# Kernel tuning notes

Measured on AMD Instinct MI355X. Metric: run time of the kernel, lower is better.

Reference implementation:

```python
import jax, jax.numpy as jnp
import numpy as np

B, C, COUT, L, K = 16, 64, 64, 16384, 3
STRIDE, PAD, DIL, G, DG = 1, 1, 1, 1, 1
LOUT = (L + 2 * PAD - DIL * (K - 1) - 1) // STRIDE + 1


def _conv1d(x, w, b, pad, groups):
    # x: [B, Cin, L], w: [Cout, Cin/groups, k] (torch Conv1d layout)
    y = jax.lax.conv_general_dilated(
        x, w, window_strides=(1,), padding=[(pad, pad)],
        dimension_numbers=('NCH', 'OIH', 'NCH'), feature_group_count=groups)
    return y + b[None, :, None]


def setup_inputs() -> dict:
    key = jax.random.key(0)
    k = jax.random.split(key, 11)
    s = jnp.float32(0.02)  # module init: normal(0, 0.02)
    return {
        'x': jax.random.normal(k[0], (B, C, L), jnp.float32),
        'w_off_dw': jax.random.normal(k[1], (C, 1, 7), jnp.float32) * s,
        'b_off_dw': jax.random.normal(k[2], (C,), jnp.float32) * s,
        'w_off_pw': jax.random.normal(k[3], (G * DG * K, C, 1), jnp.float32) * s,
        'b_off_pw': jax.random.normal(k[4], (G * DG * K,), jnp.float32) * s,
        'w_msk_dw': jax.random.normal(k[5], (C, 1, 7), jnp.float32) * s,
        'b_msk_dw': jax.random.normal(k[6], (C,), jnp.float32) * s,
        'w_msk_pw': jax.random.normal(k[7], (G * DG * K, C, 1), jnp.float32) * s,
        'b_msk_pw': jax.random.normal(k[8], (G * DG * K,), jnp.float32) * s,
        'weight': jax.random.normal(k[9], (COUT, C // G, K), jnp.float32) * s,
        'bias': jax.random.normal(k[10], (COUT,), jnp.float32) * s,
    }


def _deform_conv1d(x, w_off_dw, b_off_dw, w_off_pw, b_off_pw,
                   w_msk_dw, b_msk_dw, w_msk_pw, b_msk_pw, weight, bias):
    # offset / modulation-mask branches: depthwise k=7 conv -> 1x1 conv
    offset = _conv1d(_conv1d(x, w_off_dw, b_off_dw, 3, C), w_off_pw, b_off_pw, 0, 1)  # [B, G*DG*K, Lout]
    mask = jax.nn.sigmoid(_conv1d(_conv1d(x, w_msk_dw, b_msk_dw, 3, C), w_msk_pw, b_msk_pw, 0, 1))

    cpd = C // (G * DG)  # channels per deformable group
    off = jnp.repeat(offset.reshape(B, G * DG, K, LOUT), cpd, axis=1)  # [B, C, K, Lout]
    msk = jnp.repeat(mask.reshape(B, G * DG, K, LOUT), cpd, axis=1)

    base = jnp.arange(LOUT, dtype=x.dtype) * STRIDE - PAD  # [Lout]
    kpos = jnp.arange(K, dtype=x.dtype) * DIL              # [K]
    p = base[None, :] + kpos[:, None]                       # [K, Lout]
    p = p[None, None] + off                                 # fractional sample positions [B, C, K, Lout]

    i0 = jnp.floor(p)
    frac = p - i0
    i0i = i0.astype(jnp.int32)
    i1i = i0i + 1

    xb = jnp.broadcast_to(x[:, :, None, :], (B, C, K, L))
    x0 = jnp.take_along_axis(xb, jnp.clip(i0i, 0, L - 1), axis=-1)
    x1 = jnp.take_along_axis(xb, jnp.clip(i1i, 0, L - 1), axis=-1)
    v0 = ((i0i >= 0) & (i0i < L)).astype(x.dtype)  # zero padding outside
    v1 = ((i1i >= 0) & (i1i < L)).astype(x.dtype)

    # linear interpolation + mask modulation
    val = ((1.0 - frac) * x0 * v0 + frac * x1 * v1) * msk  # [B, C, K, Lout]

    # grouped contraction over (in-channels-per-group, kernel taps)
    out = jnp.einsum('bgikl,goik->bgol',
                     val.reshape(B, G, C // G, K, LOUT),
                     weight.reshape(G, COUT // G, C // G, K))
    return out.reshape(B, COUT, LOUT) + bias[None, :, None]


def reference(x, w_off_dw, b_off_dw, w_off_pw, b_off_pw,
              w_msk_dw, b_msk_dw, w_msk_pw, b_msk_pw, weight, bias):
    return _deform_conv1d(x, w_off_dw, b_off_dw, w_off_pw, b_off_pw,
                          w_msk_dw, b_msk_dw, w_msk_pw, b_msk_pw, weight, bias)
```

## Files before the change

kernel.cpp:

```cpp
#include <hip/hip_runtime.h>
#include <cstdint>

#define LX 16384
#define NB 16
#define LT 64
#define HALO 8
#define XI (LT + 2*HALO)
#define XPD 36
#define HPD 36

typedef __attribute__((ext_vector_type(2))) _Float16 h2;
typedef __attribute__((ext_vector_type(8))) _Float16 h8;
typedef __attribute__((ext_vector_type(4))) unsigned u4;
typedef __attribute__((ext_vector_type(4))) float f4;

static __device__ __forceinline__ h2 u2h(unsigned u) {
    union { unsigned u; h2 h; } v; v.u = u; return v.h;
}
static __device__ __forceinline__ unsigned h2u(h2 h) {
    union { h2 h; unsigned u; } v; v.h = h; return v.u;
}
static __device__ __forceinline__ unsigned pkrtz(float a, float b) {
    auto r = __builtin_amdgcn_cvt_pkrtz(a, b);
    union { decltype(r) h; unsigned u; } v; v.h = r;
    return v.u;
}

__global__ void prep_kernel(const float* __restrict__ weight,
                            const float* __restrict__ b_off_pw, const float* __restrict__ w_off_pw,
                            const float* __restrict__ b_off_dw,
                            const float* __restrict__ b_msk_pw, const float* __restrict__ w_msk_pw,
                            const float* __restrict__ b_msk_dw,
                            const float* __restrict__ w_off_dw, const float* __restrict__ w_msk_dw,
                            short* __restrict__ A, float* __restrict__ beff,
                            unsigned* __restrict__ dwt2, unsigned* __restrict__ pwt2) {
    int bid = blockIdx.x;
    int t = threadIdx.x;
    if (bid < 48) {
        int idx = bid * 256 + t;
        int k = idx >> 12;
        int o = (idx >> 6) & 63, c = idx & 63;
        union { _Float16 h; short s; } v;
        v.h = (_Float16)weight[o * 192 + c * 3 + k];
        A[idx] = v.s;
    } else {
        for (int idx = t; idx < 448; idx += 256) {
            int br = idx / 224, r2 = idx - br * 224;
            int j = r2 >> 5, cp = r2 & 31;
            const float* src = br ? w_msk_dw : w_off_dw;
            h2 h; h[0] = (_Float16)src[(2 * cp) * 7 + j]; h[1] = (_Float16)src[(2 * cp + 1) * 7 + j];
            dwt2[idx] = h2u(h);
        }
        if (t < 192) {
            int br = t / 96, r2 = t - br * 96;
            int m = r2 >> 5, cp = r2 & 31;
            const float* src = br ? w_msk_pw : w_off_pw;
            h2 h; h[0] = (_Float16)src[m * 64 + 2 * cp]; h[1] = (_Float16)src[m * 64 + 2 * cp + 1];
            pwt2[t] = h2u(h);
        }
        if (t < 6) {
            int br = t / 3, m = t % 3;
            const float* pw = br ? w_msk_pw : w_off_pw;
            const float* bd = br ? b_msk_dw : b_off_dw;
            const float* bp = br ? b_msk_pw : b_off_pw;
            float s = bp[m];
            for (int c = 0; c < 64; ++c) s += pw[m * 64 + c] * bd[c];
            beff[t] = s;
        }
    }
}

__launch_bounds__(256, 3)
__global__ void deform_main(const float* __restrict__ x,
                            const float* __restrict__ bias,
                            const short* __restrict__ A,
                            const float* __restrict__ beff,
                            const unsigned* __restrict__ dwt2_g,
                            const unsigned* __restrict__ pwt2_g,
                            float* __restrict__ out) {
    __shared__ __align__(16) unsigned xdw[XI * XPD];
    __shared__ __align__(16) unsigned Hdw[3 * XI * HPD];
    __shared__ __align__(16) unsigned dwt2[448];
    __shared__ __align__(16) unsigned pwt2[192];
    __shared__ unsigned kl_wp[3][64];
    __shared__ int      kl_li[3][64];
    __shared__ float bias_l[64];
    __shared__ float beff_l[8];

    const int t = threadIdx.x;
    const int l0 = blockIdx.x * LT;
    const int b = blockIdx.y;

    const float* xb = x + (size_t)b * (64 * LX);
    #pragma unroll
    for (int s = 0; s < 3; ++s) {
        int p = t + 256 * s;
        if (p < 640) {
            int cp = p & 31, up = p >> 5;
            int g4 = l0 - HALO + up * 4;
            f4 v0 = {0.f, 0.f, 0.f, 0.f}, v1 = {0.f, 0.f, 0.f, 0.f};
            if ((unsigned)g4 < (unsigned)LX) {
                v0 = *(const f4*)(xb + (size_t)(2 * cp) * LX + g4);
                v1 = *(const f4*)(xb + (size_t)(2 * cp + 1) * LX + g4);
            }
            #pragma unroll
            for (int d = 0; d < 4; ++d) {
                int i = up * 4 + d;
                int pc = ((cp >> 3) + i) & 3;
                xdw[i * XPD + pc * 8 + (cp & 7)] = pkrtz(v0[d], v1[d]);
            }
        }
    }
    for (int idx = t; idx < 448; idx += 256) dwt2[idx] = dwt2_g[idx];
    if (t < 192) pwt2[t] = pwt2_g[t];
    if (t < 64) bias_l[t] = bias[t];
    if (t < 6)  beff_l[t] = beff[t];

    const int lane = t & 63;
    const int wv = t >> 6;
    const int r = lane & 15, q = lane >> 4;
    const int m0 = wv * 16;
    h8 afr[6];
    {
        const h8* Ap = (const h8*)A;
        #pragma unroll
        for (int k = 0; k < 3; ++k)
            #pragma unroll
            for (int ks = 0; ks < 2; ++ks)
                afr[k * 2 + ks] = Ap[(k * 64 + m0 + r) * 8 + ks * 4 + q];
    }
    __syncthreads();

    {
        const int l = t >> 2, cc = t & 3;
        h2 so2[8], sm2[8];
        #pragma unroll
        for (int m = 0; m < 8; ++m) { so2[m] = (h2)(_Float16)0; sm2[m] = (h2)(_Float16)0; }
        #pragma unroll
        for (int j = 0; j < 7; ++j) {
            int i = l + 5 + j;
            const unsigned* xr = &xdw[i * XPD + (((cc + i) & 3) << 3)];
            u4 xa = *(const u4*)xr;
            u4 xb2 = *(const u4*)(xr + 4);
            const unsigned* wo = &dwt2[j * 32 + cc * 8];
            const unsigned* wm = &dwt2[224 + j * 32 + cc * 8];
            u4 woa = *(const u4*)wo, wob = *(const u4*)(wo + 4);
            u4 wma = *(const u4*)wm, wmb = *(const u4*)(wm + 4);
            #pragma unroll
            for (int m = 0; m < 4; ++m) {
                so2[m]     += u2h(xa[m])  * u2h(woa[m]);
                so2[m + 4] += u2h(xb2[m]) * u2h(wob[m]);
                sm2[m]     += u2h(xa[m])  * u2h(wma[m]);
                sm2[m + 4] += u2h(xb2[m]) * u2h(wmb[m]);
            }
        }
        float po[3] = {0.f, 0.f, 0.f}, pm[3] = {0.f, 0.f, 0.f};
        #pragma unroll
        for (int m3 = 0; m3 < 3; ++m3) {
            const unsigned* p0 = &pwt2[m3 * 32 + cc * 8];
            const unsigned* p1 = &pwt2[96 + m3 * 32 + cc * 8];
            u4 a0 = *(const u4*)p0, a1 = *(const u4*)(p0 + 4);
            u4 b0 = *(const u4*)p1, b1 = *(const u4*)(p1 + 4);
            #pragma unroll
            for (int m = 0; m < 4; ++m) {
                po[m3] = __builtin_amdgcn_fdot2(so2[m],     u2h(a0[m]), po[m3], false);
                po[m3] = __builtin_amdgcn_fdot2(so2[m + 4], u2h(a1[m]), po[m3], false);
                pm[m3] = __builtin_amdgcn_fdot2(sm2[m],     u2h(b0[m]), pm[m3], false);
                pm[m3] = __builtin_amdgcn_fdot2(sm2[m + 4], u2h(b1[m]), pm[m3], false);
            }
        }
        #pragma unroll
        for (int d = 1; d <= 2; d <<= 1) {
            #pragma unroll
            for (int m3 = 0; m3 < 3; ++m3) {
                po[m3] += __shfl_xor(po[m3], d);
                pm[m3] += __shfl_xor(pm[m3], d);
            }
        }
        if (cc < 3) {
            int k = cc;
            float off = (k == 0 ? po[0] : k == 1 ? po[1] : po[2]) + beff_l[k];
            float z   = (k == 0 ? pm[0] : k == 1 ? pm[1] : pm[2]) + beff_l[3 + k];
            float msk = 1.0f / (1.0f + __expf(-z));
            float p = (float)(l0 + l - 1 + k) + off;
            float fl = floorf(p);
            int i0 = (int)fl, i1 = i0 + 1;
            float fr = p - fl;
            int li0 = i0 - l0 + HALO, li1 = li0 + 1;
            float w0 = (((unsigned)i0 < (unsigned)LX) && ((unsigned)li0 < (unsigned)XI)) ? (1.0f - fr) * msk : 0.0f;
            float w1 = (((unsigned)i1 < (unsigned)LX) && ((unsigned)li1 < (unsigned)XI)) ? fr * msk : 0.0f;
            li0 = min(max(li0, 0), XI - 2);
            kl_wp[k][l] = pkrtz(w0, w1);
            kl_li[k][l] = li0;
        }
    }

    {
        h8 bfr[10];
        #pragma unroll
        for (int n = 0; n < 5; ++n)
            #pragma unroll
            for (int ks = 0; ks < 2; ++ks) {
                int i = n * 16 + r;
                int pc = ((2 * ks + (q >> 1)) + i) & 3;
                bfr[n * 2 + ks] = *(const h8*)&xdw[i * XPD + pc * 8 + (q & 1) * 4];
            }
        #pragma unroll
        for (int k = 0; k < 3; ++k) {
            #pragma unroll
            for (int n = 0; n < 5; ++n) {
                f4 acc = {0.f, 0.f, 0.f, 0.f};
                acc = __builtin_amdgcn_mfma_f32_16x16x32_f16(afr[k * 2 + 0], bfr[n * 2 + 0], acc, 0, 0, 0);
                acc = __builtin_amdgcn_mfma_f32_16x16x32_f16(afr[k * 2 + 1], bfr[n * 2 + 1], acc, 0, 0, 0);
                int i = n * 16 + r;
                int pc = (wv + i) & 3;
                unsigned* dst = &Hdw[(k * XI + i) * HPD + pc * 8 + 2 * q];
                dst[0] = pkrtz(acc[0], acc[1]);
                dst[1] = pkrtz(acc[2], acc[3]);
            }
        }
    }
    __syncthreads();

    {
        const int l = t & 63, og = t >> 6;
        float acc[16];
        #pragma unroll
        for (int oi = 0; oi < 16; ++oi) acc[oi] = bias_l[og * 16 + oi];
        #pragma unroll
        for (int k = 0; k < 3; ++k) {
            h2 wph = u2h(kl_wp[k][l]);
            int li0 = kl_li[k][l];
            int b0 = (k * XI + li0) * HPD + (((og + li0) & 3) << 3);
            int b1 = (k * XI + li0 + 1) * HPD + (((og + li0 + 1) & 3) << 3);
            u4 r0a = *(const u4*)&Hdw[b0], r0b = *(const u4*)&Hdw[b0 + 4];
            u4 r1a = *(const u4*)&Hdw[b1], r1b = *(const u4*)&Hdw[b1 + 4];
            #pragma unroll
            for (int m = 0; m < 4; ++m) {
                unsigned dA0 = __builtin_amdgcn_perm(r1a[m], r0a[m], 0x05040100u);
                unsigned dA1 = __builtin_amdgcn_perm(r1a[m], r0a[m], 0x07060302u);
                acc[2 * m]     = __builtin_amdgcn_fdot2(u2h(dA0), wph, acc[2 * m], false);
                acc[2 * m + 1] = __builtin_amdgcn_fdot2(u2h(dA1), wph, acc[2 * m + 1], false);
                unsigned dB0 = __builtin_amdgcn_perm(r1b[m], r0b[m], 0x05040100u);
                unsigned dB1 = __builtin_amdgcn_perm(r1b[m], r0b[m], 0x07060302u);
                acc[8 + 2 * m]     = __builtin_amdgcn_fdot2(u2h(dB0), wph, acc[8 + 2 * m], false);
                acc[8 + 2 * m + 1] = __builtin_amdgcn_fdot2(u2h(dB1), wph, acc[8 + 2 * m + 1], false);
            }
        }
        float* ob = out + ((size_t)b * 64 + og * 16) * LX + l0 + l;
        #pragma unroll
        for (int oi = 0; oi < 16; ++oi) ob[(size_t)oi * LX] = acc[oi];
    }
}

extern "C" void kernel_launch(void* const* d_in, const int* in_sizes, int n_in,
                              void* d_out, int out_size, void* d_ws, size_t ws_size,
                              hipStream_t stream) {
    const float* x        = (const float*)d_in[0];
    const float* w_off_dw = (const float*)d_in[1];
    const float* b_off_dw = (const float*)d_in[2];
    const float* w_off_pw = (const float*)d_in[3];
    const float* b_off_pw = (const float*)d_in[4];
    const float* w_msk_dw = (const float*)d_in[5];
    const float* b_msk_dw = (const float*)d_in[6];
    const float* w_msk_pw = (const float*)d_in[7];
    const float* b_msk_pw = (const float*)d_in[8];
    const float* weight   = (const float*)d_in[9];
    const float* bias     = (const float*)d_in[10];
    float* out = (float*)d_out;

    short*    A    = (short*)d_ws;
    float*    beff = (float*)((char*)d_ws + 24576);
    unsigned* dwt2 = (unsigned*)((char*)d_ws + 24608);
    unsigned* pwt2 = (unsigned*)((char*)d_ws + 26400);

    hipLaunchKernelGGL(prep_kernel, dim3(49), dim3(256), 0, stream,
                       weight, b_off_pw, w_off_pw, b_off_dw, b_msk_pw, w_msk_pw, b_msk_dw,
                       w_off_dw, w_msk_dw, A, beff, dwt2, pwt2);
    hipLaunchKernelGGL(deform_main, dim3(LX / LT, NB), dim3(256), 0, stream,
                       x, bias, A, beff, dwt2, pwt2, out);
}
```

Measured before the change: 158.2 us.

## Interpolate input before MFMA contraction instead of gathering precomputed per-tap products

Reorders the computation so each lane first bilinearly interpolates and mask-weights the x samples (in fp16) for its output column and tap. A single K=192 MFMA contraction over (channel, tap) then produces the outputs directly. The old path computed weight·x for every tap over the whole halo tile, stored it in a large shared H buffer, and gathered and interpolated it with fdot2. Dropping that buffer cuts LDS use, which is why the launch bound now asks for 5 blocks per CU instead of 3. The costs are fp16 interpolation arithmetic, which loses some precision, and A fragments that are now read from global memory inside the MFMA loop.

Measured after the change: 179.4 us. 13.4% more time.

```diff
diff --git a/kernel.cpp b/kernel.cpp
--- a/kernel.cpp
+++ b/kernel.cpp
@@ -7,7 +7,6 @@
 #define HALO 8
 #define XI (LT + 2*HALO)
 #define XPD 36
-#define HPD 36
 
 typedef __attribute__((ext_vector_type(2))) _Float16 h2;
 typedef __attribute__((ext_vector_type(8))) _Float16 h8;
@@ -32,17 +31,18 @@
                             const float* __restrict__ b_msk_pw, const float* __restrict__ w_msk_pw,
                             const float* __restrict__ b_msk_dw,
                             const float* __restrict__ w_off_dw, const float* __restrict__ w_msk_dw,
-                            short* __restrict__ A, float* __restrict__ beff,
+                            short* __restrict__ A2, float* __restrict__ beff,
                             unsigned* __restrict__ dwt2, unsigned* __restrict__ pwt2) {
     int bid = blockIdx.x;
     int t = threadIdx.x;
     if (bid < 48) {
         int idx = bid * 256 + t;
-        int k = idx >> 12;
-        int o = (idx >> 6) & 63, c = idx & 63;
+        int o = idx / 192;
+        int rem = idx - o * 192;
+        int tap = rem >> 6, c = rem & 63;
         union { _Float16 h; short s; } v;
-        v.h = (_Float16)weight[o * 192 + c * 3 + k];
-        A[idx] = v.s;
+        v.h = (_Float16)weight[o * 192 + c * 3 + tap];
+        A2[idx] = v.s;
     } else {
         for (int idx = t; idx < 448; idx += 256) {
             int br = idx / 224, r2 = idx - br * 224;
@@ -70,16 +70,15 @@
     }
 }
 
-__launch_bounds__(256, 3)
+__launch_bounds__(256, 5)
 __global__ void deform_main(const float* __restrict__ x,
                             const float* __restrict__ bias,
-                            const short* __restrict__ A,
+                            const short* __restrict__ A2,
                             const float* __restrict__ beff,
                             const unsigned* __restrict__ dwt2_g,
                             const unsigned* __restrict__ pwt2_g,
                             float* __restrict__ out) {
     __shared__ __align__(16) unsigned xdw[XI * XPD];
-    __shared__ __align__(16) unsigned Hdw[3 * XI * HPD];
     __shared__ __align__(16) unsigned dwt2[448];
     __shared__ __align__(16) unsigned pwt2[192];
     __shared__ unsigned kl_wp[3][64];
@@ -115,20 +114,6 @@
     if (t < 192) pwt2[t] = pwt2_g[t];
     if (t < 64) bias_l[t] = bias[t];
     if (t < 6)  beff_l[t] = beff[t];
-
-    const int lane = t & 63;
-    const int wv = t >> 6;
-    const int r = lane & 15, q = lane >> 4;
-    const int m0 = wv * 16;
-    h8 afr[6];
-    {
-        const h8* Ap = (const h8*)A;
-        #pragma unroll
-        for (int k = 0; k < 3; ++k)
-            #pragma unroll
-            for (int ks = 0; ks < 2; ++ks)
-                afr[k * 2 + ks] = Ap[(k * 64 + m0 + r) * 8 + ks * 4 + q];
-    }
     __syncthreads();
 
     {
@@ -194,62 +179,51 @@
             kl_li[k][l] = li0;
         }
     }
+    __syncthreads();
 
     {
-        h8 bfr[10];
-        #pragma unroll
-        for (int n = 0; n < 5; ++n)
-            #pragma unroll
-            for (int ks = 0; ks < 2; ++ks) {
-                int i = n * 16 + r;
-                int pc = ((2 * ks + (q >> 1)) + i) & 3;
-                bfr[n * 2 + ks] = *(const h8*)&xdw[i * XPD + pc * 8 + (q & 1) * 4];
-            }
-        #pragma unroll
-        for (int k = 0; k < 3; ++k) {
-            #pragma unroll
-            for (int n = 0; n < 5; ++n) {
-                f4 acc = {0.f, 0.f, 0.f, 0.f};
-                acc = __builtin_amdgcn_mfma_f32_16x16x32_f16(afr[k * 2 + 0], bfr[n * 2 + 0], acc, 0, 0, 0);
-                acc = __builtin_amdgcn_mfma_f32_16x16x32_f16(afr[k * 2 + 1], bfr[n * 2 + 1], acc, 0, 0, 0);
-                int i = n * 16 + r;
-                int pc = (wv + i) & 3;
-                unsigned* dst = &Hdw[(k * XI + i) * HPD + pc * 8 + 2 * q];
-                dst[0] = pkrtz(acc[0], acc[1]);
-                dst[1] = pkrtz(acc[2], acc[3]);
-            }
-        }
-    }
-    __syncthreads();
-
-    {
-        const int l = t & 63, og = t >> 6;
-        float acc[16];
-        #pragma unroll
-        for (int oi = 0; oi < 16; ++oi) acc[oi] = bias_l[og * 16 + oi];
-        #pragma unroll
-        for (int k = 0; k < 3; ++k) {
-            h2 wph = u2h(kl_wp[k][l]);
-            int li0 = kl_li[k][l];
-            int b0 = (k * XI + li0) * HPD + (((og + li0) & 3) << 3);
-            int b1 = (k * XI + li0 + 1) * HPD + (((og + li0 + 1) & 3) << 3);
-            u4 r0a = *(const u4*)&Hdw[b0], r0b = *(const u4*)&Hdw[b0 + 4];
-            u4 r1a = *(const u4*)&Hdw[b1], r1b = *(const u4*)&Hdw[b1 + 4];
-            #pragma unroll
-            for (int m = 0; m < 4; ++m) {
-                unsigned dA0 = __builtin_amdgcn_perm(r1a[m], r0a[m], 0x05040100u);
-                unsigned dA1 = __builtin_amdgcn_perm(r1a[m], r0a[m], 0x07060302u);
-                acc[2 * m]     = __builtin_amdgcn_fdot2(u2h(dA0), wph, acc[2 * m], false);
-                acc[2 * m + 1] = __builtin_amdgcn_fdot2(u2h(dA1), wph, acc[2 * m + 1], false);
-                unsigned dB0 = __builtin_amdgcn_perm(r1b[m], r0b[m], 0x05040100u);
-                unsigned dB1 = __builtin_amdgcn_perm(r1b[m], r0b[m], 0x07060302u);
-                acc[8 + 2 * m]     = __builtin_amdgcn_fdot2(u2h(dB0), wph, acc[8 + 2 * m], false);
-                acc[8 + 2 * m + 1] = __builtin_amdgcn_fdot2(u2h(dB1), wph, acc[8 + 2 * m + 1], false);
-            }
-        }
-        float* ob = out + ((size_t)b * 64 + og * 16) * LX + l0 + l;
-        #pragma unroll
-        for (int oi = 0; oi < 16; ++oi) ob[(size_t)oi * LX] = acc[oi];
+        const int lane = t & 63;
+        const int wv = t >> 6;
+        const int r = lane & 15, q = lane >> 4;
+        const int lcol = wv * 16 + r;
+
+        h8 bfr[6];
+        #pragma unroll
+        for (int kk = 0; kk < 6; ++kk) {
+            const int tap = kk >> 1;
+            unsigned wp = kl_wp[tap][lcol];
+            unsigned w00 = __builtin_amdgcn_perm(wp, wp, 0x01000100u);
+            unsigned w11 = __builtin_amdgcn_perm(wp, wp, 0x03020302u);
+            int li0 = kl_li[tap][lcol];
+            int cp0 = (((kk & 1) << 5) + (q << 3)) >> 1;
+            int chunkL = cp0 >> 3;
+            int o0 = li0 * XPD + ((((chunkL + li0) & 3) << 3) | (cp0 & 7));
+            int o1 = (li0 + 1) * XPD + ((((chunkL + li0 + 1) & 3) << 3) | (cp0 & 7));
+            u4 r0 = *(const u4*)&xdw[o0];
+            u4 r1 = *(const u4*)&xdw[o1];
+            u4 xs;
+            #pragma unroll
+            for (int d = 0; d < 4; ++d)
+                xs[d] = h2u(u2h(r0[d]) * u2h(w00) + u2h(r1[d]) * u2h(w11));
+            union { u4 u; h8 h; } cvt; cvt.u = xs;
+            bfr[kk] = cvt.h;
+        }
+
+        const h8* Ap = (const h8*)A2;
+        #pragma unroll
+        for (int mt = 0; mt < 4; ++mt) {
+            f4 acc = {0.f, 0.f, 0.f, 0.f};
+            #pragma unroll
+            for (int kk = 0; kk < 6; ++kk) {
+                h8 af = Ap[(mt * 16 + r) * 24 + kk * 4 + q];
+                acc = __builtin_amdgcn_mfma_f32_16x16x32_f16(af, bfr[kk], acc, 0, 0, 0);
+            }
+            int ob = mt * 16 + 4 * q;
+            float* op = out + ((size_t)b * 64 + ob) * LX + l0 + lcol;
+            #pragma unroll
+            for (int e = 0; e < 4; ++e)
+                op[(size_t)e * LX] = acc[e] + bias_l[ob + e];
+        }
     }
 }
 
@@ -269,14 +243,14 @@
     const float* bias     = (const float*)d_in[10];
     float* out = (float*)d_out;
 
-    short*    A    = (short*)d_ws;
+    short*    A2   = (short*)d_ws;
     float*    beff = (float*)((char*)d_ws + 24576);
     unsigned* dwt2 = (unsigned*)((char*)d_ws + 24608);
     unsigned* pwt2 = (unsigned*)((char*)d_ws + 26400);
 
     hipLaunchKernelGGL(prep_kernel, dim3(49), dim3(256), 0, stream,
                        weight, b_off_pw, w_off_pw, b_off_dw, b_msk_pw, w_msk_pw, b_msk_dw,
-                       w_off_dw, w_msk_dw, A, beff, dwt2, pwt2);
+                       w_off_dw, w_msk_dw, A2, beff, dwt2, pwt2);
     hipLaunchKernelGGL(deform_main, dim3(LX / LT, NB), dim3(256), 0, stream,
-                       x, bias, A, beff, dwt2, pwt2, out);
-}
+                       x, bias, A2, beff, dwt2, pwt2, out);
+}
```
